# Kernel optimization log

Hardware: AMD Instinct MI355X
Metric: run time of the kernel (lower is better)

## Reference

```python
import jax, jax.numpy as jnp
import numpy as np

BN_EPS = 1e-5

def setup_inputs() -> dict:
    key = jax.random.key(0)
    ks = jax.random.split(key, 12)
    B, N, C, D = 8, 2048, 768, 384  # batch, tokens, high_dim, low_dim//reduc_ratio
    s_in = 1.0 / np.sqrt(C)
    s_out = 1.0 / np.sqrt(D)
    return {
        "x_h": jax.random.normal(ks[0], (B, N, C), jnp.float32),
        "x_l": jax.random.normal(ks[1], (B, N, C), jnp.float32),
        "w_g": jax.random.normal(ks[2], (D, C), jnp.float32) * s_in,
        "b_g": jax.random.normal(ks[3], (D,), jnp.float32) * s_in,
        "w_theta": jax.random.normal(ks[4], (D, C), jnp.float32) * s_in,
        "b_theta": jax.random.normal(ks[5], (D,), jnp.float32) * s_in,
        "w_phi": jax.random.normal(ks[6], (D, C), jnp.float32) * s_in,
        "b_phi": jax.random.normal(ks[7], (D,), jnp.float32) * s_in,
        "w_out": jax.random.normal(ks[8], (C, D), jnp.float32) * s_out,
        "b_out": jax.random.normal(ks[9], (C,), jnp.float32) * s_out,
        "bn_gamma": jax.random.normal(ks[10], (C,), jnp.float32),
        "bn_beta": jax.random.normal(ks[11], (C,), jnp.float32),
    }

def reference(x_h, x_l, w_g, b_g, w_theta, b_theta, w_phi, b_phi, w_out, b_out, bn_gamma, bn_beta):
    # 1x1 conv1d over channels == per-token linear
    g_x = jnp.einsum('bnc,dc->bnd', x_l, w_g) + b_g          # [B, N_l, D]
    theta_x = jnp.einsum('bnc,dc->bnd', x_h, w_theta) + b_theta  # [B, N_h, D]
    phi_x = jnp.einsum('bnc,dc->bnd', x_l, w_phi) + b_phi    # [B, N_l, D]
    n_l = phi_x.shape[1]
    energy = jnp.einsum('bnd,bmd->bnm', theta_x, phi_x)      # [B, N_h, N_l]
    attention = energy / n_l                                  # scalar normalization
    y = jnp.einsum('bnm,bmd->bnd', attention, g_x)           # [B, N_h, D]
    y = jnp.einsum('bnd,cd->bnc', y, w_out) + b_out          # [B, N_h, C]
    # BatchNorm1d (training mode): per-channel stats over batch and length dims
    mean = jnp.mean(y, axis=(0, 1))
    var = jnp.var(y, axis=(0, 1))
    y = bn_gamma * (y - mean) * jax.lax.rsqrt(var + BN_EPS) + bn_beta
    return y + x_h                                            # [B, N_h, C]
```

## Files before the change

### kernel.cpp

```cpp
#include <hip/hip_runtime.h>

typedef short bf16x8 __attribute__((ext_vector_type(8)));
typedef float f32x4 __attribute__((ext_vector_type(4)));

constexpr int Bb = 8, Ntok = 2048, Cdim = 768, Ddim = 384, Mrows = 16384;

__device__ __forceinline__ void gload16(const void* g, void* l) {
    __builtin_amdgcn_global_load_lds(
        (const __attribute__((address_space(1))) unsigned int*)g,
        (__attribute__((address_space(3))) unsigned int*)l, 16, 0, 0);
}

__device__ __forceinline__ unsigned short f2bf(float x) {
    union { float f; unsigned u; } c; c.f = x;
    const unsigned r = c.u + 0x7fffu + ((c.u >> 16) & 1u);
    return (unsigned short)(r >> 16);
}
__device__ __forceinline__ float bf2f(unsigned short u) {
    union { unsigned u; float f; } c; c.u = (unsigned)u << 16;
    return c.f;
}
__device__ __forceinline__ uint4 cvt8(const float4 a, const float4 b) {
    union { unsigned short u[8]; uint4 q; } r;
    r.u[0] = f2bf(a.x); r.u[1] = f2bf(a.y); r.u[2] = f2bf(a.z); r.u[3] = f2bf(a.w);
    r.u[4] = f2bf(b.x); r.u[5] = f2bf(b.y); r.u[6] = f2bf(b.z); r.u[7] = f2bf(b.w);
    return r.q;
}

__device__ __forceinline__ void fence_acq() {
    __builtin_amdgcn_s_barrier();
    asm volatile("" ::: "memory");
    __builtin_amdgcn_sched_barrier(0);
}
__device__ __forceinline__ void fence_rel() {
    __builtin_amdgcn_sched_barrier(0);
    asm volatile("s_waitcnt lgkmcnt(0)" ::: "memory");
    __builtin_amdgcn_s_barrier();
}

__device__ __forceinline__ void swz_xcd(int& bx, int& by, int& bz) {
    const int NN = gridDim.x, NY = gridDim.y;
    const int NP = NY * gridDim.z;
    const int lin = blockIdx.x + NN * (blockIdx.y + NY * blockIdx.z);
    const int x = lin & 7, g = lin >> 3;
    const int pan = x * (NP >> 3) + g / NN;
    bx = g % NN; by = pan % NY; bz = pan / NY;
}

__global__ __launch_bounds__(256) void cast_w(const float* __restrict__ s0, const float* __restrict__ s1,
                                              const float* __restrict__ s2, const float* __restrict__ s3,
                                              unsigned short* __restrict__ d0, unsigned short* __restrict__ d1,
                                              unsigned short* __restrict__ d2, unsigned short* __restrict__ d3) {
    constexpr int n8 = 294912 / 8;
    const int i = blockIdx.x * 256 + threadIdx.x;
    const int sel = i / n8, loc = i - sel * n8;
    const float* s = sel == 0 ? s0 : sel == 1 ? s1 : sel == 2 ? s2 : s3;
    unsigned short* d = sel == 0 ? d0 : sel == 1 ? d1 : sel == 2 ? d2 : d3;
    const float4* s4 = (const float4*)s;
    ((uint4*)d)[loc] = cvt8(s4[2 * loc], s4[2 * loc + 1]);
}

template <int OMODE, bool SPLITK, bool AFP32>
__global__ __launch_bounds__(256) void gemm_bf16(
        const void* __restrict__ Abase_, long sA,
        const unsigned short* __restrict__ Bbase, long sB,
        const float* __restrict__ bias, const float* __restrict__ bias2, int Nsplit,
        void* __restrict__ Cbase, long sC,
        int M, int N, int K, float scale,
        float* __restrict__ psumG, float* __restrict__ psqG) {
    constexpr int SMEM_BYTES = (OMODE == 2) ? 34304 : 32768;
    __shared__ __align__(16) char smem[SMEM_BYTES];

    int bxi, byi, bzi;
    swz_xcd(bxi, byi, bzi);

    const int tid  = threadIdx.x;
    const int lane = tid & 63;
    const int w    = tid >> 6;
    const int wm   = w >> 1, wn = w & 1;
    const int bm = byi * 128, bn = bxi * 128;
    const int zz = bzi;

    int zb, kStart, kEnd;
    if constexpr (SPLITK) {
        zb = zz >> 2;
        const int kl = K >> 2;
        kStart = (zz & 3) * kl;
        kEnd = kStart + kl;
    } else {
        zb = zz; kStart = 0; kEnd = K;
    }

    const unsigned short* B = Bbase + (size_t)zb * sB;
    const float* Af = (const float*)Abase_ + (AFP32 ? (size_t)zb * sA : 0);
    const unsigned short* Ah = (const unsigned short*)Abase_ + (AFP32 ? 0 : (size_t)zb * sA);

    const int ldRow = tid >> 2;
    const int ldK   = (tid & 3) * 8;
    const unsigned ldsOff = tid * 16;
    const size_t aOff0 = (size_t)(bm + ldRow) * K + ldK;
    const size_t aOff1 = (size_t)(bm + 64 + ldRow) * K + ldK;
    const size_t bOff0 = (size_t)(bn + ldRow) * K + ldK;
    const size_t bOff1 = (size_t)(bn + 64 + ldRow) * K + ldK;

    f32x4 acc[4][4] = {};
    const int fr = lane & 15;
    const int fh = (lane >> 4) * 16;

    float4 na0, na1, na2, na3;

    auto stageB = [&](int p, int k0) {
        char* s = smem + 16384 + p * 8192;
        gload16(B + bOff0 + k0, s + ldsOff);
        gload16(B + bOff1 + k0, s + 4096 + ldsOff);
    };
    auto stageA_g = [&](int p, int k0) {
        char* s = smem + p * 8192;
        gload16(Ah + aOff0 + k0, s + ldsOff);
        gload16(Ah + aOff1 + k0, s + 4096 + ldsOff);
    };
    auto loadA_f = [&](int k0) {
        na0 = *(const float4*)(Af + aOff0 + k0);
        na1 = *(const float4*)(Af + aOff0 + k0 + 4);
        na2 = *(const float4*)(Af + aOff1 + k0);
        na3 = *(const float4*)(Af + aOff1 + k0 + 4);
    };
    auto writeA_f = [&](int p) {
        char* s = smem + p * 8192;
        *(uint4*)(s + ldsOff)        = cvt8(na0, na1);
        *(uint4*)(s + 4096 + ldsOff) = cvt8(na2, na3);
    };

    if constexpr (AFP32) {
        loadA_f(kStart);
        stageB(0, kStart);
        writeA_f(0);
    } else {
        stageA_g(0, kStart);
        stageB(0, kStart);
    }

    int it = 0;
    for (int k0 = kStart; k0 < kEnd; k0 += 32, ++it) {
        const int p = it & 1;
        const bool more = (k0 + 32 < kEnd);
        if (more) {
            if constexpr (AFP32) { loadA_f(k0 + 32); stageB(p ^ 1, k0 + 32); }
            else { stageA_g(p ^ 1, k0 + 32); stageB(p ^ 1, k0 + 32); }
        }
        if (more) {
            if constexpr (AFP32) asm volatile("s_waitcnt vmcnt(6)" ::: "memory");
            else                 asm volatile("s_waitcnt vmcnt(4)" ::: "memory");
        } else {
            asm volatile("s_waitcnt vmcnt(0)" ::: "memory");
        }
        asm volatile("s_waitcnt lgkmcnt(0)" ::: "memory");
        fence_acq();
        const char* smA = smem + p * 8192;
        const char* smB = smem + 16384 + p * 8192;
        bf16x8 fa[4], fb[4];
#pragma unroll
        for (int m = 0; m < 4; ++m)
            fa[m] = *(const bf16x8*)(smA + (wm * 64 + m * 16 + fr) * 64 + fh);
#pragma unroll
        for (int n = 0; n < 4; ++n)
            fb[n] = *(const bf16x8*)(smB + (wn * 64 + n * 16 + fr) * 64 + fh);
#pragma unroll
        for (int m = 0; m < 4; ++m)
#pragma unroll
            for (int n = 0; n < 4; ++n)
                acc[m][n] = __builtin_amdgcn_mfma_f32_16x16x32_bf16(fa[m], fb[n], acc[m][n], 0, 0, 0);
        if constexpr (AFP32) {
            if (more) writeA_f(p ^ 1);
        }
        fence_rel();
    }

    const int r0 = (lane >> 4) * 4;
    const int cc = lane & 15;
    auto getbias = [&](int gcol) -> float {
        if (!bias) return 0.0f;
        return gcol < Nsplit ? bias[gcol] : bias2[gcol - Nsplit];
    };

    if constexpr (OMODE == 0) {
        float* C = (float*)Cbase + (size_t)(SPLITK ? zz : zb) * sC;
#pragma unroll
        for (int n = 0; n < 4; ++n) {
            const int col = bn + wn * 64 + n * 16 + cc;
            const float bv = getbias(col);
#pragma unroll
            for (int m = 0; m < 4; ++m)
#pragma unroll
                for (int j = 0; j < 4; ++j)
                    C[(size_t)(bm + wm * 64 + m * 16 + r0 + j) * N + col] = acc[m][n][j] + bv;
        }
    } else if constexpr (OMODE == 1) {
        unsigned short* C = (unsigned short*)Cbase + (size_t)zb * sC;
#pragma unroll
        for (int n = 0; n < 4; ++n) {
            const int col = bn + wn * 64 + n * 16 + cc;
            const float bv = getbias(col);
#pragma unroll
            for (int m = 0; m < 4; ++m)
#pragma unroll
                for (int j = 0; j < 4; ++j)
                    C[(size_t)(bm + wm * 64 + m * 16 + r0 + j) * N + col] =
                        f2bf(acc[m][n][j] * scale + bv);
        }
    } else if constexpr (OMODE == 2) {
        unsigned short* T = (unsigned short*)smem;
#pragma unroll
        for (int n = 0; n < 4; ++n) {
            const int ccol = wn * 64 + n * 16 + cc;
            const float bv = getbias(bn + ccol);
#pragma unroll
            for (int m = 0; m < 4; ++m)
#pragma unroll
                for (int j = 0; j < 4; ++j)
                    T[ccol * 134 + (wm * 64 + m * 16 + r0 + j)] = f2bf(acc[m][n][j] + bv);
        }
        __syncthreads();
        const int b   = bm >> 11;
        const int bmb = bm & 2047;
        unsigned short* Co = (unsigned short*)Cbase + (size_t)b * N * Ntok;
#pragma unroll
        for (int i = 0; i < 32; ++i) {
            const int d = w * 32 + i;
            const unsigned v = *(const unsigned*)((const char*)smem + d * 268 + lane * 4);
            *(unsigned*)(Co + (size_t)(bn + d) * Ntok + bmb + lane * 2) = v;
        }
    } else {
        unsigned short* C = (unsigned short*)Cbase + (size_t)zb * sC;
        float colS[4], colQ[4];
#pragma unroll
        for (int n = 0; n < 4; ++n) {
            const int col = bn + wn * 64 + n * 16 + cc;
            const float bv = getbias(col);
            float s = 0.f, q = 0.f;
#pragma unroll
            for (int m = 0; m < 4; ++m)
#pragma unroll
                for (int j = 0; j < 4; ++j) {
                    const float v = acc[m][n][j] + bv;
                    C[(size_t)(bm + wm * 64 + m * 16 + r0 + j) * N + col] = f2bf(v);
                    s += v; q = fmaf(v, v, q);
                }
            s += __shfl_xor(s, 16); s += __shfl_xor(s, 32);
            q += __shfl_xor(q, 16); q += __shfl_xor(q, 32);
            colS[n] = s; colQ[n] = q;
        }
        float* sums = (float*)smem;
        float* sqs  = sums + 256;
        if (lane < 16) {
#pragma unroll
            for (int n = 0; n < 4; ++n) {
                sums[wm * 128 + wn * 64 + n * 16 + cc] = colS[n];
                sqs [wm * 128 + wn * 64 + n * 16 + cc] = colQ[n];
            }
        }
        __syncthreads();
        if (tid < 128) {
            const int slot = zb * gridDim.y + byi;
            psumG[(size_t)slot * Cdim + bn + tid] = sums[tid] + sums[128 + tid];
            psqG [(size_t)slot * Cdim + bn + tid] = sqs[tid]  + sqs[128 + tid];
        }
    }
}

__global__ __launch_bounds__(256) void reduce_mt(const float* __restrict__ part,
                                                 unsigned short* __restrict__ Mo) {
    const int i = blockIdx.x * 256 + threadIdx.x;
    const int e = i * 4;
    const int b = e / (Ddim * Ddim);
    const int r = e - b * (Ddim * Ddim);
    const float* base = part + (size_t)b * 4 * (Ddim * Ddim) + r;
    float4 s = *(const float4*)(base);
    const float4 s1 = *(const float4*)(base + 1 * Ddim * Ddim);
    const float4 s2 = *(const float4*)(base + 2 * Ddim * Ddim);
    const float4 s3 = *(const float4*)(base + 3 * Ddim * Ddim);
    s.x += s1.x + s2.x + s3.x; s.y += s1.y + s2.y + s3.y;
    s.z += s1.z + s2.z + s3.z; s.w += s1.w + s2.w + s3.w;
    constexpr float sc = 1.0f / (float)Ntok;
    union { unsigned short u[4]; uint2 q; } o;
    o.u[0] = f2bf(s.x * sc); o.u[1] = f2bf(s.y * sc);
    o.u[2] = f2bf(s.z * sc); o.u[3] = f2bf(s.w * sc);
    *(uint2*)(Mo + e) = o.q;
}

__global__ __launch_bounds__(256) void bn_finalize(const float* __restrict__ psum,
                                                   const float* __restrict__ psq,
                                                   const float* __restrict__ gamma,
                                                   const float* __restrict__ beta,
                                                   float* __restrict__ a,
                                                   float* __restrict__ bb) {
    const int c = blockIdx.x * 256 + threadIdx.x;
    if (c >= Cdim) return;
    float s = 0.f, q = 0.f;
    for (int b = 0; b < 128; ++b) { s += psum[(size_t)b * Cdim + c]; q += psq[(size_t)b * Cdim + c]; }
    const float mean = s * (1.0f / (float)Mrows);
    const float var  = fmaf(-mean, mean, q * (1.0f / (float)Mrows));
    const float inv  = rsqrtf(var + 1e-5f);
    const float gsc  = gamma[c] * inv;
    a[c]  = gsc;
    bb[c] = fmaf(-mean, gsc, beta[c]);
}

__global__ __launch_bounds__(256) void bn_apply(const unsigned short* __restrict__ y,
                                                const float* __restrict__ xh,
                                                const float* __restrict__ a,
                                                const float* __restrict__ bb,
                                                float* __restrict__ outp) {
    const size_t i = (size_t)blockIdx.x * 256 + threadIdx.x;
    union { uint4 q; unsigned short u[8]; } v; v.q = ((const uint4*)y)[i];
    const int c8 = (int)(i % (Cdim / 8));
    const float4 A0 = ((const float4*)a)[c8 * 2],  A1 = ((const float4*)a)[c8 * 2 + 1];
    const float4 B0 = ((const float4*)bb)[c8 * 2], B1 = ((const float4*)bb)[c8 * 2 + 1];
    const float4 X0 = ((const float4*)xh)[i * 2],  X1 = ((const float4*)xh)[i * 2 + 1];
    float4 o0, o1;
    o0.x = fmaf(A0.x, bf2f(v.u[0]), B0.x) + X0.x;
    o0.y = fmaf(A0.y, bf2f(v.u[1]), B0.y) + X0.y;
    o0.z = fmaf(A0.z, bf2f(v.u[2]), B0.z) + X0.z;
    o0.w = fmaf(A0.w, bf2f(v.u[3]), B0.w) + X0.w;
    o1.x = fmaf(A1.x, bf2f(v.u[4]), B1.x) + X1.x;
    o1.y = fmaf(A1.y, bf2f(v.u[5]), B1.y) + X1.y;
    o1.z = fmaf(A1.z, bf2f(v.u[6]), B1.z) + X1.z;
    o1.w = fmaf(A1.w, bf2f(v.u[7]), B1.w) + X1.w;
    ((float4*)outp)[i * 2]     = o0;
    ((float4*)outp)[i * 2 + 1] = o1;
}

extern "C" void kernel_launch(void* const* d_in, const int* in_sizes, int n_in,
                              void* d_out, int out_size, void* d_ws, size_t ws_size,
                              hipStream_t stream) {
    const float* x_h   = (const float*)d_in[0];
    const float* x_l   = (const float*)d_in[1];
    const float* w_g   = (const float*)d_in[2];
    const float* b_g   = (const float*)d_in[3];
    const float* w_th  = (const float*)d_in[4];
    const float* b_th  = (const float*)d_in[5];
    const float* w_ph  = (const float*)d_in[6];
    const float* b_ph  = (const float*)d_in[7];
    const float* w_out = (const float*)d_in[8];
    const float* b_out = (const float*)d_in[9];
    const float* gamma = (const float*)d_in[10];
    const float* beta  = (const float*)d_in[11];
    float* out = (float*)d_out;

    char* p = (char*)d_ws;
    unsigned short* Scr   = (unsigned short*)p; p += (size_t)Mrows * Cdim * 2;
    unsigned short* Wth16 = (unsigned short*)p; p += 294912 * 2;
    unsigned short* Wpg16 = (unsigned short*)p; p += 2 * 294912 * 2;
    unsigned short* Wout16= (unsigned short*)p; p += 294912 * 2;
    unsigned short* Tbuf  = (unsigned short*)p; p += (size_t)Mrows * Ddim * 2;
    unsigned short* PGT   = (unsigned short*)p; p += (size_t)Mrows * Cdim * 2;
    unsigned short* Mbuf  = (unsigned short*)p; p += (size_t)Bb * Ddim * Ddim * 2;
    unsigned short* QTbuf = (unsigned short*)p; p += (size_t)Bb * Cdim * Ddim * 2;
    float* psum = (float*)p; p += (size_t)128 * Cdim * 4;
    float* psq  = (float*)p; p += (size_t)128 * Cdim * 4;
    float* avec = (float*)p; p += Cdim * 4;
    float* bvec = (float*)p; p += Cdim * 4;
    float* part = (float*)Scr;
    unsigned short* Ybuf = Scr;

    dim3 blk(256);
    const int BIG = 1 << 30;

    cast_w<<<576, blk, 0, stream>>>(w_th, w_ph, w_g, w_out,
                                    Wth16, Wpg16, Wpg16 + 294912, Wout16);
    gemm_bf16<1, false, true><<<dim3(3, 128, 1), blk, 0, stream>>>(
        x_h, 0, Wth16, 0, b_th, nullptr, BIG, Tbuf, 0, Mrows, Ddim, Cdim, 1.0f,
        nullptr, nullptr);
    gemm_bf16<2, false, true><<<dim3(6, 128, 1), blk, 0, stream>>>(
        x_l, 0, Wpg16, 0, b_ph, b_g, Ddim, PGT, 0, Mrows, 2 * Ddim, Cdim, 1.0f,
        nullptr, nullptr);
    gemm_bf16<0, true, false><<<dim3(3, 3, 32), blk, 0, stream>>>(
        PGT, (long)2 * Ddim * Ntok,
        PGT + (size_t)Ddim * Ntok, (long)2 * Ddim * Ntok, nullptr, nullptr, BIG,
        part, (long)Ddim * Ddim, Ddim, Ddim, Ntok, 1.0f, nullptr, nullptr);
    reduce_mt<<<1152, blk, 0, stream>>>(part, Mbuf);
    gemm_bf16<1, false, false><<<dim3(3, 6, 8), blk, 0, stream>>>(
        Wout16, 0, Mbuf, (long)Ddim * Ddim, nullptr, nullptr, BIG,
        QTbuf, (long)Cdim * Ddim, Cdim, Ddim, Ddim, 1.0f, nullptr, nullptr);
    gemm_bf16<3, false, false><<<dim3(6, 16, 8), blk, 0, stream>>>(
        Tbuf, (long)Ntok * Ddim, QTbuf, (long)Cdim * Ddim, b_out, nullptr, BIG,
        Ybuf, (long)Ntok * Cdim, Ntok, Cdim, Ddim, 1.0f, psum, psq);
    bn_finalize<<<dim3(3), blk, 0, stream>>>(psum, psq, gamma, beta, avec, bvec);
    bn_apply<<<dim3(6144), blk, 0, stream>>>(Ybuf, x_h, avec, bvec, out);
}
```

Before: 146.3 us.

## Triple-buffer GEMM LDS pipeline with two-tile-ahead prefetch

Replaces the double-buffered K loop with a three-stage LDS ring, so global loads for tile t+2 are in flight while tile t is computed. The fp32-A path alternates two register sets and is unrolled by two, and the bf16 path drops the extra LDS-count wait on release. LDS usage grows to 48 KB per block, which can lower occupancy, and the hand-tuned vmcnt counts must match the number of outstanding loads exactly.

```diff
diff --git a/kernel.cpp b/kernel.cpp
--- a/kernel.cpp
+++ b/kernel.cpp
@@ -27,16 +27,13 @@
     return r.q;
 }
 
-__device__ __forceinline__ void fence_acq() {
-    __builtin_amdgcn_s_barrier();
-    asm volatile("" ::: "memory");
-    __builtin_amdgcn_sched_barrier(0);
-}
-__device__ __forceinline__ void fence_rel() {
-    __builtin_amdgcn_sched_barrier(0);
-    asm volatile("s_waitcnt lgkmcnt(0)" ::: "memory");
-    __builtin_amdgcn_s_barrier();
-}
+#define ACQ()  do { __builtin_amdgcn_s_barrier(); asm volatile("" ::: "memory"); \
+                    __builtin_amdgcn_sched_barrier(0); } while (0)
+#define RELW() do { __builtin_amdgcn_sched_barrier(0); \
+                    asm volatile("s_waitcnt lgkmcnt(0)" ::: "memory"); \
+                    __builtin_amdgcn_s_barrier(); } while (0)
+#define RELN() do { __builtin_amdgcn_sched_barrier(0); \
+                    __builtin_amdgcn_s_barrier(); } while (0)
 
 __device__ __forceinline__ void swz_xcd(int& bx, int& by, int& bz) {
     const int NN = gridDim.x, NY = gridDim.y;
@@ -68,8 +65,7 @@
         void* __restrict__ Cbase, long sC,
         int M, int N, int K, float scale,
         float* __restrict__ psumG, float* __restrict__ psqG) {
-    constexpr int SMEM_BYTES = (OMODE == 2) ? 34304 : 32768;
-    __shared__ __align__(16) char smem[SMEM_BYTES];
+    __shared__ __align__(16) char smem[49152];
 
     int bxi, byi, bzi;
     swz_xcd(bxi, byi, bzi);
@@ -90,6 +86,7 @@
     } else {
         zb = zz; kStart = 0; kEnd = K;
     }
+    const int nt = (kEnd - kStart) >> 5;
 
     const unsigned short* B = Bbase + (size_t)zb * sB;
     const float* Af = (const float*)Abase_ + (AFP32 ? (size_t)zb * sA : 0);
@@ -107,57 +104,43 @@
     const int fr = lane & 15;
     const int fh = (lane >> 4) * 16;
 
-    float4 na0, na1, na2, na3;
-
-    auto stageB = [&](int p, int k0) {
-        char* s = smem + 16384 + p * 8192;
-        gload16(B + bOff0 + k0, s + ldsOff);
-        gload16(B + bOff1 + k0, s + 4096 + ldsOff);
-    };
-    auto stageA_g = [&](int p, int k0) {
-        char* s = smem + p * 8192;
-        gload16(Ah + aOff0 + k0, s + ldsOff);
-        gload16(Ah + aOff1 + k0, s + 4096 + ldsOff);
-    };
-    auto loadA_f = [&](int k0) {
-        na0 = *(const float4*)(Af + aOff0 + k0);
-        na1 = *(const float4*)(Af + aOff0 + k0 + 4);
-        na2 = *(const float4*)(Af + aOff1 + k0);
-        na3 = *(const float4*)(Af + aOff1 + k0 + 4);
-    };
-    auto writeA_f = [&](int p) {
-        char* s = smem + p * 8192;
-        *(uint4*)(s + ldsOff)        = cvt8(na0, na1);
-        *(uint4*)(s + 4096 + ldsOff) = cvt8(na2, na3);
-    };
-
-    if constexpr (AFP32) {
-        loadA_f(kStart);
-        stageB(0, kStart);
-        writeA_f(0);
-    } else {
-        stageA_g(0, kStart);
-        stageB(0, kStart);
-    }
-
-    int it = 0;
-    for (int k0 = kStart; k0 < kEnd; k0 += 32, ++it) {
-        const int p = it & 1;
-        const bool more = (k0 + 32 < kEnd);
-        if (more) {
-            if constexpr (AFP32) { loadA_f(k0 + 32); stageB(p ^ 1, k0 + 32); }
-            else { stageA_g(p ^ 1, k0 + 32); stageB(p ^ 1, k0 + 32); }
-        }
-        if (more) {
-            if constexpr (AFP32) asm volatile("s_waitcnt vmcnt(6)" ::: "memory");
-            else                 asm volatile("s_waitcnt vmcnt(4)" ::: "memory");
-        } else {
-            asm volatile("s_waitcnt vmcnt(0)" ::: "memory");
-        }
-        asm volatile("s_waitcnt lgkmcnt(0)" ::: "memory");
-        fence_acq();
-        const char* smA = smem + p * 8192;
-        const char* smB = smem + 16384 + p * 8192;
+    auto bufA = [&](int p) -> char* { return smem + p * 8192; };
+    auto bufB = [&](int p) -> char* { return smem + 24576 + p * 8192; };
+
+    auto stageB = [&](int p, int t) {
+        const int k0 = kStart + t * 32;
+        gload16(B + bOff0 + k0, bufB(p) + ldsOff);
+        gload16(B + bOff1 + k0, bufB(p) + 4096 + ldsOff);
+    };
+    auto stageA_g = [&](int p, int t) {
+        const int k0 = kStart + t * 32;
+        gload16(Ah + aOff0 + k0, bufA(p) + ldsOff);
+        gload16(Ah + aOff1 + k0, bufA(p) + 4096 + ldsOff);
+    };
+
+    float4 a00, a01, a02, a03, a10, a11, a12, a13;
+    auto loadA0 = [&](int t) {
+        const int k0 = kStart + t * 32;
+        a00 = *(const float4*)(Af + aOff0 + k0); a01 = *(const float4*)(Af + aOff0 + k0 + 4);
+        a02 = *(const float4*)(Af + aOff1 + k0); a03 = *(const float4*)(Af + aOff1 + k0 + 4);
+    };
+    auto loadA1 = [&](int t) {
+        const int k0 = kStart + t * 32;
+        a10 = *(const float4*)(Af + aOff0 + k0); a11 = *(const float4*)(Af + aOff0 + k0 + 4);
+        a12 = *(const float4*)(Af + aOff1 + k0); a13 = *(const float4*)(Af + aOff1 + k0 + 4);
+    };
+    auto writeA0 = [&](int p) {
+        *(uint4*)(bufA(p) + ldsOff)        = cvt8(a00, a01);
+        *(uint4*)(bufA(p) + 4096 + ldsOff) = cvt8(a02, a03);
+    };
+    auto writeA1 = [&](int p) {
+        *(uint4*)(bufA(p) + ldsOff)        = cvt8(a10, a11);
+        *(uint4*)(bufA(p) + 4096 + ldsOff) = cvt8(a12, a13);
+    };
+
+    auto compute = [&](int p) {
+        const char* smA = bufA(p);
+        const char* smB = bufB(p);
         bf16x8 fa[4], fb[4];
 #pragma unroll
         for (int m = 0; m < 4; ++m)
@@ -170,10 +153,57 @@
 #pragma unroll
             for (int n = 0; n < 4; ++n)
                 acc[m][n] = __builtin_amdgcn_mfma_f32_16x16x32_bf16(fa[m], fb[n], acc[m][n], 0, 0, 0);
-        if constexpr (AFP32) {
-            if (more) writeA_f(p ^ 1);
-        }
-        fence_rel();
+    };
+
+    if constexpr (AFP32) {
+        loadA0(0); stageB(0, 0);
+        loadA1(1); stageB(1, 1);
+        writeA0(0);
+        asm volatile("s_waitcnt lgkmcnt(0)" ::: "memory");
+        int p = 0;
+        for (int t = 0; t + 2 < nt; t += 2) {
+            int p1 = p + 1; if (p1 == 3) p1 = 0;
+            int p2 = p1 + 1; if (p2 == 3) p2 = 0;
+            loadA0(t + 2); stageB(p2, t + 2);
+            asm volatile("s_waitcnt vmcnt(12)" ::: "memory");
+            ACQ();
+            compute(p);
+            writeA1(p1);
+            RELW();
+            loadA1(t + 3); stageB(p, t + 3);
+            asm volatile("s_waitcnt vmcnt(12)" ::: "memory");
+            ACQ();
+            compute(p1);
+            writeA0(p2);
+            RELW();
+            p = p2;
+        }
+        int p1 = p + 1; if (p1 == 3) p1 = 0;
+        asm volatile("s_waitcnt vmcnt(6)" ::: "memory");
+        ACQ();
+        compute(p);
+        writeA1(p1);
+        RELW();
+        asm volatile("s_waitcnt vmcnt(0)" ::: "memory");
+        ACQ();
+        compute(p1);
+        RELN();
+    } else {
+        stageA_g(0, 0); stageB(0, 0);
+        stageA_g(1, 1); stageB(1, 1);
+        int p = 0;
+        for (int t = 0; t < nt; ++t) {
+            int p2 = p + 2; if (p2 >= 3) p2 -= 3;
+            const bool m2 = (t + 2) < nt;
+            if (m2) { stageA_g(p2, t + 2); stageB(p2, t + 2); }
+            if (m2)                asm volatile("s_waitcnt vmcnt(8)" ::: "memory");
+            else if (t + 1 < nt)   asm volatile("s_waitcnt vmcnt(4)" ::: "memory");
+            else                   asm volatile("s_waitcnt vmcnt(0)" ::: "memory");
+            ACQ();
+            compute(p);
+            RELN();
+            p = p + 1 == 3 ? 0 : p + 1;
+        }
     }
 
     const int r0 = (lane >> 4) * 4;
```

Result: slower. 161.2 us (+10.2%).
